# Performance work log

Hardware: AMD Instinct MI355X
Metric: run time of the kernel (lower is better)

The kernel has to match this reference:

```python
import jax, jax.numpy as jnp
import numpy as np

MATRIX_SIZE = 448
DIAGONAL_OFFSET = 2
# number of upper-triangular entries with offset 2
UT_LEN = (MATRIX_SIZE - DIAGONAL_OFFSET) * (MATRIX_SIZE - DIAGONAL_OFFSET + 1) // 2  # 99681


def setup_inputs() -> dict:
    key = jax.random.key(0)
    kx, kb = jax.random.split(key)
    x = jax.random.normal(kx, (16, 32, UT_LEN), dtype=jnp.float32)
    reverse_bool = jax.random.randint(kb, (16,), 0, 2).astype(jnp.bool_)
    return {"x": x, "reverse_bool": reverse_bool}


def reference(x, reverse_bool):
    # Conditionally reverse the upper-triangular (flattened) axis per batch item.
    # Original torch code flips x[b] along the last dim where reverse_bool[b] is True.
    flipped = jnp.flip(x, axis=-1)
    return jnp.where(reverse_bool[:, None, None], flipped, x)
```

## Files before the change

kernel.cpp:

```cpp
#include <hip/hip_runtime.h>


#define L_DIM 99681
#define C_DIM 32
#define B_DIM 16
#define CL (C_DIM * L_DIM)
#define N_ELEM (B_DIM * CL)
#define N4 (N_ELEM / 4)

__global__ __launch_bounds__(256) void SwitchReverseTriu_kernel(
    const float* __restrict__ x,
    const int* __restrict__ rev,
    float* __restrict__ out)
{
    const float4* __restrict__ x4 = reinterpret_cast<const float4*>(x);
    float4* __restrict__ o4 = reinterpret_cast<float4*>(out);

    const int stride = gridDim.x * blockDim.x;
    for (int f4 = blockIdx.x * blockDim.x + threadIdx.x; f4 < N4; f4 += stride) {
        const int e0 = f4 * 4;
        const int b  = e0 / CL;
        const int m  = e0 - b * CL;

        if (rev[b]) {
            int c = m / L_DIM;
            int i = m - c * L_DIM;
            const float* __restrict__ xb = x + b * CL;
            float v0, v1, v2, v3;
            {
                if (i == L_DIM) { i = 0; ++c; }
                v0 = xb[c * L_DIM + (L_DIM - 1 - i)]; ++i;
                if (i == L_DIM) { i = 0; ++c; }
                v1 = xb[c * L_DIM + (L_DIM - 1 - i)]; ++i;
                if (i == L_DIM) { i = 0; ++c; }
                v2 = xb[c * L_DIM + (L_DIM - 1 - i)]; ++i;
                if (i == L_DIM) { i = 0; ++c; }
                v3 = xb[c * L_DIM + (L_DIM - 1 - i)];
            }
            o4[f4] = make_float4(v0, v1, v2, v3);
        } else {
            o4[f4] = x4[f4];
        }
    }
}

extern "C" void kernel_launch(void* const* d_in, const int* in_sizes, int n_in,
                              void* d_out, int out_size, void* d_ws, size_t ws_size,
                              hipStream_t stream) {
    const float* x  = (const float*)d_in[0];
    const int* rev  = (const int*)d_in[1];
    float* out      = (float*)d_out;

    const int threads = 256;
    const int blocks  = 2048;
    SwitchReverseTriu_kernel<<<blocks, threads, 0, stream>>>(x, rev, out);
}
```

Baseline: 78.66 us.

## Restructure reverse as per-row blocks with aligned float4 loads and LDS reversal

Assigns four blocks to each (batch, channel) row and lets each block check the reverse flag once, so the per-element division and branching go away. Reversed rows load aligned float4 chunks into shared memory and write the reversed float4 back. Alignment is fixed per row, and the unaligned head and tail elements are handled separately. This adds LDS traffic and a grid of only 2048 blocks, each looping over about 24 chunks.

```diff
diff --git a/kernel.cpp b/kernel.cpp
--- a/kernel.cpp
+++ b/kernel.cpp
@@ -1,45 +1,72 @@
 #include <hip/hip_runtime.h>
 
 
-#define L_DIM 99681
-#define C_DIM 32
-#define B_DIM 16
-#define CL (C_DIM * L_DIM)
-#define N_ELEM (B_DIM * CL)
-#define N4 (N_ELEM / 4)
+#define L_DIM  99681
+#define B_DIM  16
+#define C_DIM  32
+#define NROWS  (B_DIM * C_DIM)
+#define NTOT   (NROWS * L_DIM)
+#define BPR    4
+#define NFULL  97
 
 __global__ __launch_bounds__(256) void SwitchReverseTriu_kernel(
     const float* __restrict__ x,
     const int* __restrict__ rev,
     float* __restrict__ out)
 {
-    const float4* __restrict__ x4 = reinterpret_cast<const float4*>(x);
-    float4* __restrict__ o4 = reinterpret_cast<float4*>(out);
+    __shared__ float lds[4][264];
 
-    const int stride = gridDim.x * blockDim.x;
-    for (int f4 = blockIdx.x * blockDim.x + threadIdx.x; f4 < N4; f4 += stride) {
-        const int e0 = f4 * 4;
-        const int b  = e0 / CL;
-        const int m  = e0 - b * CL;
+    const int blk = blockIdx.x;
+    const int row = blk >> 2;
+    const int bir = blk & (BPR - 1);
+    const int b   = row >> 5;
+    const int O   = row * L_DIM;
+    const int a   = (4 - (row & 3)) & 3;
+    const bool r  = rev[b] != 0;
 
-        if (rev[b]) {
-            int c = m / L_DIM;
-            int i = m - c * L_DIM;
-            const float* __restrict__ xb = x + b * CL;
-            float v0, v1, v2, v3;
-            {
-                if (i == L_DIM) { i = 0; ++c; }
-                v0 = xb[c * L_DIM + (L_DIM - 1 - i)]; ++i;
-                if (i == L_DIM) { i = 0; ++c; }
-                v1 = xb[c * L_DIM + (L_DIM - 1 - i)]; ++i;
-                if (i == L_DIM) { i = 0; ++c; }
-                v2 = xb[c * L_DIM + (L_DIM - 1 - i)]; ++i;
-                if (i == L_DIM) { i = 0; ++c; }
-                v3 = xb[c * L_DIM + (L_DIM - 1 - i)];
+    const int t = threadIdx.x;
+
+    if (!r) {
+        for (int ch = bir; ch < NFULL; ch += BPR) {
+            const int g = O + a + ch * 1024 + 4 * t;
+            *reinterpret_cast<float4*>(out + g) =
+                *reinterpret_cast<const float4*>(x + g);
+        }
+    } else {
+        const int w = t >> 6;
+        const int j = t & 63;
+        float* Lw = lds[w];
+        for (int ch = bir; ch < NFULL; ch += BPR) {
+            const int i0w = a + ch * 1024 + (w << 8);
+            const int R   = O + L_DIM - 256 - i0w;
+            const int d   = R & 3;
+            const int RA  = R - d;
+
+            float4 v = *reinterpret_cast<const float4*>(x + RA + 4 * j);
+            *reinterpret_cast<float4*>(Lw + 4 * j) = v;
+            if (j == 0 && d) {
+                #pragma unroll
+                for (int k = 0; k < 4; ++k) {
+                    const int idx = RA + 256 + k;
+                    Lw[256 + k] = (idx < NTOT) ? x[idx] : 0.0f;
+                }
             }
-            o4[f4] = make_float4(v0, v1, v2, v3);
-        } else {
-            o4[f4] = x4[f4];
+            const int q = d + 255 - 4 * j;
+            float4 o;
+            o.x = Lw[q];
+            o.y = Lw[q - 1];
+            o.z = Lw[q - 2];
+            o.w = Lw[q - 3];
+            const int g = O + i0w + 4 * j;
+            *reinterpret_cast<float4*>(out + g) = o;
+        }
+    }
+
+    if (bir == 0) {
+        for (int i2 = t; i2 < 353; i2 += 256) {
+            const int ii  = (i2 < a) ? i2 : i2 + NFULL * 1024;
+            const int src = r ? (L_DIM - 1 - ii) : ii;
+            out[O + ii] = x[O + src];
         }
     }
 }
@@ -51,7 +78,5 @@
     const int* rev  = (const int*)d_in[1];
     float* out      = (float*)d_out;
 
-    const int threads = 256;
-    const int blocks  = 2048;
-    SwitchReverseTriu_kernel<<<blocks, threads, 0, stream>>>(x, rev, out);
+    SwitchReverseTriu_kernel<<<NROWS * BPR, 256, 0, stream>>>(x, rev, out);
 }
```

Result: slower. 106.2 us (+35.0%).

## Vectorize reversed reads, load reverse mask via ballot, unroll grid-stride loop 4x

Applied to the files above, without the earlier changes.

Reversed rows are now read with one 16-byte load from the mirrored offset and permuted in registers, where before they took four scalar gathers. A slow scalar path remains for the rare groups that straddle a channel boundary. The per-batch reverse flags are collapsed into a 16-bit mask with a wavefront ballot, so the loop no longer loads rev[b] on every iteration. The grid-stride loop is unrolled 4x so several loads are in flight before the stores. The mirrored loads are misaligned whenever L_DIM is not a multiple of 4, which may split them across cache lines.

```diff
diff --git a/kernel.cpp b/kernel.cpp
--- a/kernel.cpp
+++ b/kernel.cpp
@@ -1,46 +1,86 @@
 #include <hip/hip_runtime.h>
 
 
-#define L_DIM 99681
-#define C_DIM 32
-#define B_DIM 16
-#define CL (C_DIM * L_DIM)
+#define L_DIM  99681
+#define B_DIM  16
+#define C_DIM  32
+#define CL     (C_DIM * L_DIM)
 #define N_ELEM (B_DIM * CL)
-#define N4 (N_ELEM / 4)
+#define N4     (N_ELEM / 4)
+
+__device__ __forceinline__ float4 process_one(
+    const float* __restrict__ x, unsigned mask16, int f4)
+{
+    const unsigned e0 = (unsigned)f4 * 4u;
+    const unsigned b  = e0 / CL;
+    const unsigned m  = e0 - b * CL;
+    const unsigned c  = m / L_DIM;
+    const unsigned i  = m - c * L_DIM;
+    const bool r      = (mask16 >> b) & 1u;
+    const int chanBase = (int)(b * CL + c * L_DIM);
+
+    int roff = L_DIM - 4 - (int)i;
+    roff = roff < 0 ? 0 : roff;
+    const int src = chanBase + (r ? roff : (int)i);
+
+    float u[4];
+    __builtin_memcpy(u, x + src, 16);
+
+    float4 o;
+    o.x = r ? u[3] : u[0];
+    o.y = r ? u[2] : u[1];
+    o.z = r ? u[1] : u[2];
+    o.w = r ? u[0] : u[3];
+
+    if (__builtin_expect(r && (int)i > L_DIM - 4, 0)) {
+        float v0, v1, v2, v3;
+        {
+            unsigned mk = m + 0, ck = mk / L_DIM, ik = mk - ck * L_DIM;
+            v0 = x[b * CL + ck * L_DIM + (L_DIM - 1 - ik)];
+        }
+        {
+            unsigned mk = m + 1, ck = mk / L_DIM, ik = mk - ck * L_DIM;
+            v1 = x[b * CL + ck * L_DIM + (L_DIM - 1 - ik)];
+        }
+        {
+            unsigned mk = m + 2, ck = mk / L_DIM, ik = mk - ck * L_DIM;
+            v2 = x[b * CL + ck * L_DIM + (L_DIM - 1 - ik)];
+        }
+        {
+            unsigned mk = m + 3, ck = mk / L_DIM, ik = mk - ck * L_DIM;
+            v3 = x[b * CL + ck * L_DIM + (L_DIM - 1 - ik)];
+        }
+        o = make_float4(v0, v1, v2, v3);
+    }
+    return o;
+}
 
 __global__ __launch_bounds__(256) void SwitchReverseTriu_kernel(
     const float* __restrict__ x,
     const int* __restrict__ rev,
     float* __restrict__ out)
 {
-    const float4* __restrict__ x4 = reinterpret_cast<const float4*>(x);
-    float4* __restrict__ o4 = reinterpret_cast<float4*>(out);
+    const int lane = threadIdx.x & 63;
+    const int rv = rev[lane & 15];
+    const unsigned long long bal = __ballot(rv != 0);
+    const unsigned mask16 = (unsigned)(bal & 0xFFFFull);
 
-    const int stride = gridDim.x * blockDim.x;
-    for (int f4 = blockIdx.x * blockDim.x + threadIdx.x; f4 < N4; f4 += stride) {
-        const int e0 = f4 * 4;
-        const int b  = e0 / CL;
-        const int m  = e0 - b * CL;
+    const int S = gridDim.x * blockDim.x;
+    int f4 = blockIdx.x * blockDim.x + threadIdx.x;
 
-        if (rev[b]) {
-            int c = m / L_DIM;
-            int i = m - c * L_DIM;
-            const float* __restrict__ xb = x + b * CL;
-            float v0, v1, v2, v3;
-            {
-                if (i == L_DIM) { i = 0; ++c; }
-                v0 = xb[c * L_DIM + (L_DIM - 1 - i)]; ++i;
-                if (i == L_DIM) { i = 0; ++c; }
-                v1 = xb[c * L_DIM + (L_DIM - 1 - i)]; ++i;
-                if (i == L_DIM) { i = 0; ++c; }
-                v2 = xb[c * L_DIM + (L_DIM - 1 - i)]; ++i;
-                if (i == L_DIM) { i = 0; ++c; }
-                v3 = xb[c * L_DIM + (L_DIM - 1 - i)];
-            }
-            o4[f4] = make_float4(v0, v1, v2, v3);
-        } else {
-            o4[f4] = x4[f4];
-        }
+    for (; f4 + 3 * S < N4; f4 += 4 * S) {
+        float4 o0 = process_one(x, mask16, f4);
+        float4 o1 = process_one(x, mask16, f4 + S);
+        float4 o2 = process_one(x, mask16, f4 + 2 * S);
+        float4 o3 = process_one(x, mask16, f4 + 3 * S);
+        *reinterpret_cast<float4*>(out + (size_t)(f4)         * 4) = o0;
+        *reinterpret_cast<float4*>(out + (size_t)(f4 + S)     * 4) = o1;
+        *reinterpret_cast<float4*>(out + (size_t)(f4 + 2 * S) * 4) = o2;
+        *reinterpret_cast<float4*>(out + (size_t)(f4 + 3 * S) * 4) = o3;
+    }
+    for (; f4 < N4; f4 += S) {
+        float4 o = process_one(x, mask16, f4);
+        *reinterpret_cast<float4*>(out + (size_t)f4 * 4) = o;
     }
 }
 
@@ -51,7 +91,5 @@
     const int* rev  = (const int*)d_in[1];
     float* out      = (float*)d_out;
 
-    const int threads = 256;
-    const int blocks  = 2048;
-    SwitchReverseTriu_kernel<<<blocks, threads, 0, stream>>>(x, rev, out);
+    SwitchReverseTriu_kernel<<<2048, 256, 0, stream>>>(x, rev, out);
 }
```

New measurement: 84.91 us. +7.9%, slower.
